# Performance work log

Measured on AMD Instinct MI355X. Metric: run time of the kernel, lower is better.

## Reference

```python
import jax, jax.numpy as jnp
import numpy as np

H = 16          # num_heads
DK = 64         # k_dim_head
DV = 64         # v_dim_head
DIM = 1024      # model dim (= H*DK = H*DV)


def _split_heads(x, h):
    # ... T (H d) -> ... H T d
    x = x.reshape(x.shape[:-1] + (h, -1))
    return jnp.swapaxes(x, -2, -3)


def _merge_heads(x):
    # ... H T d -> ... T (H d)
    x = jnp.swapaxes(x, -2, -3)
    return x.reshape(x.shape[:-2] + (-1,))


def setup_inputs() -> dict:
    key = jax.random.key(0)
    ks = jax.random.split(key, 8)
    B, T = 2, 2048
    q = jax.random.normal(ks[0], (B, T, DIM), dtype=jnp.float32)
    k = jax.random.normal(ks[1], (B, T, DIM), dtype=jnp.float32)
    v = jax.random.normal(ks[2], (B, T, DIM), dtype=jnp.float32)
    # causal boolean mask [T, T] (True = attend)
    mask = jnp.tril(jnp.ones((T, T), dtype=bool))
    s = 1.0 / np.sqrt(DIM)
    # weights stored as [in, out] so projection is x @ W (== torch Linear, no bias)
    Wq = jax.random.normal(ks[3], (DIM, H * DK), dtype=jnp.float32) * s
    Wk = jax.random.normal(ks[4], (DIM, H * DK), dtype=jnp.float32) * s
    Wv = jax.random.normal(ks[5], (DIM, H * DV), dtype=jnp.float32) * s
    Wo = jax.random.normal(ks[6], (H * DV, DIM), dtype=jnp.float32) * s
    return {"q": q, "k": k, "v": v, "mask": mask,
            "Wq": Wq, "Wk": Wk, "Wv": Wv, "Wo": Wo}


def reference(q, k, v, mask, Wq, Wk, Wv, Wo):
    q_i = _split_heads(q @ Wq, H)                       # ... H T dk
    k_i = _split_heads(k @ Wk, H)                       # ... H T dk
    v_i = _split_heads(v @ Wv, H)                       # ... H T dv
    s_qk = jnp.einsum('...hik,...hjk->...hij', q_i, k_i) / jnp.sqrt(
        jnp.asarray(DK, dtype=q_i.dtype))               # ... H T T
    neg = -jnp.finfo(s_qk.dtype).max
    s_qk = jnp.where(mask, s_qk, neg)
    attn = jax.nn.softmax(s_qk, axis=-1)
    vals = jnp.einsum('...hij,...hjv->...hiv', attn, v_i)
    return _merge_heads(vals) @ Wo                      # ... T out_dim
```

## Files before the change

### kernel.cpp

```cpp
#include <hip/hip_runtime.h>
#include <hip/hip_bf16.h>
#include <stdint.h>

#define T_SEQ  2048
#define DMODEL 1024
#define NBATCH 2
#define NHEAD  16
#define DHEAD  64
#define MTOT   (NBATCH * T_SEQ)

typedef __attribute__((ext_vector_type(8))) short short8_t;
typedef __attribute__((ext_vector_type(4))) float f32x4;

typedef const __attribute__((address_space(1))) void* gas_t;
typedef __attribute__((address_space(3))) void* las_t;

__device__ __forceinline__ ushort f2bf(float f) {
    union { float f; uint32_t u; } cv; cv.f = f;
    uint32_t u = cv.u;
    return (ushort)((u + 0x7FFFu + ((u >> 16) & 1u)) >> 16);
}

__global__ __launch_bounds__(256) void convert_qkv_kernel(
        const float* __restrict__ q, const float* __restrict__ k,
        const float* __restrict__ v, ushort* __restrict__ outb) {
    const size_t per = (size_t)MTOT * DMODEL / 4;
    size_t idx = (size_t)blockIdx.x * 256 + threadIdx.x;
    int t = (int)(idx / per);
    size_t i = idx - (size_t)t * per;
    const float4* src = (const float4*)(t == 0 ? q : (t == 1 ? k : v));
    float4 val = src[i];
    ushort4 o;
    o.x = f2bf(val.x); o.y = f2bf(val.y); o.z = f2bf(val.z); o.w = f2bf(val.w);
    ((ushort4*)outb)[(size_t)t * per + i] = o;
}

__global__ __launch_bounds__(256) void convw_kernel(
        const float* __restrict__ Wq, const float* __restrict__ Wk,
        const float* __restrict__ Wv, const float* __restrict__ Wo,
        ushort* __restrict__ wt) {
    __shared__ float tile[32][33];
    int z = blockIdx.z;
    const float* W = z == 0 ? Wq : z == 1 ? Wk : z == 2 ? Wv : Wo;
    const float sc = (z == 0) ? 0.125f : 1.0f;
    ushort* out = wt + (size_t)z * DMODEL * DMODEL;
    int tx = threadIdx.x, ty = threadIdx.y;
    int k0 = blockIdx.x * 32, n0 = blockIdx.y * 32;
    #pragma unroll
    for (int i = 0; i < 4; i++)
        tile[ty + i * 8][tx] = W[(size_t)(k0 + ty + i * 8) * DMODEL + n0 + tx];
    __syncthreads();
    #pragma unroll
    for (int i = 0; i < 4; i++)
        out[(size_t)(n0 + ty + i * 8) * DMODEL + k0 + tx] = f2bf(tile[tx][ty + i * 8] * sc);
}

template <bool OUT_F32>
__global__ __launch_bounds__(256, 2) void gemm_bt_kernel(
        const ushort* __restrict__ Aall, const ushort* __restrict__ Btall,
        void* __restrict__ Call, int M, int N, int K) {
    const ushort* A  = Aall  + (size_t)blockIdx.z * M * K;
    const ushort* Bt = Btall + (size_t)blockIdx.z * N * K;

    __shared__ ushort As[128 * 32];
    __shared__ ushort Bs[128 * 32];

    const int tid  = threadIdx.x;
    const int lane = tid & 63;
    const int wid  = tid >> 6;
    const int wr = wid >> 1, wc = wid & 1;
    const int m_base = blockIdx.x * 128;
    const int n_base = blockIdx.y * 128;

    f32x4 acc[4][4] = {};

    const int srow = lane >> 2;
    const int scol = (lane & 3) * 8;

    for (int kk = 0; kk < K; kk += 32) {
        __syncthreads();
        #pragma unroll
        for (int i = 0; i < 2; i++) {
            int c = wid * 2 + i;
            const ushort* ga = A  + (size_t)(m_base + c * 16 + srow) * K + kk + scol;
            const ushort* gb = Bt + (size_t)(n_base + c * 16 + srow) * K + kk + scol;
            __builtin_amdgcn_global_load_lds((gas_t)ga, (las_t)(As + c * 512), 16, 0, 0);
            __builtin_amdgcn_global_load_lds((gas_t)gb, (las_t)(Bs + c * 512), 16, 0, 0);
        }
        __syncthreads();
        short8_t a[4], b[4];
        #pragma unroll
        for (int mt = 0; mt < 4; mt++)
            a[mt] = *(const short8_t*)(As + (wr * 64 + mt * 16 + (lane & 15)) * 32 + (lane >> 4) * 8);
        #pragma unroll
        for (int nt = 0; nt < 4; nt++)
            b[nt] = *(const short8_t*)(Bs + (wc * 64 + nt * 16 + (lane & 15)) * 32 + (lane >> 4) * 8);
        #pragma unroll
        for (int mt = 0; mt < 4; mt++)
            #pragma unroll
            for (int nt = 0; nt < 4; nt++)
                acc[mt][nt] = __builtin_amdgcn_mfma_f32_16x16x32_bf16(a[mt], b[nt], acc[mt][nt], 0, 0, 0);
    }

    const int row0 = m_base + wr * 64 + (lane >> 4) * 4;
    const int col0 = n_base + wc * 64 + (lane & 15);
    if constexpr (OUT_F32) {
        float* C = (float*)Call + (size_t)blockIdx.z * M * N;
        #pragma unroll
        for (int mt = 0; mt < 4; mt++)
            #pragma unroll
            for (int nt = 0; nt < 4; nt++)
                #pragma unroll
                for (int r = 0; r < 4; r++)
                    C[(size_t)(row0 + mt * 16 + r) * N + col0 + nt * 16] = acc[mt][nt][r];
    } else {
        ushort* C = (ushort*)Call + (size_t)blockIdx.z * M * N;
        #pragma unroll
        for (int mt = 0; mt < 4; mt++)
            #pragma unroll
            for (int nt = 0; nt < 4; nt++)
                #pragma unroll
                for (int r = 0; r < 4; r++)
                    C[(size_t)(row0 + mt * 16 + r) * N + col0 + nt * 16] = f2bf(acc[mt][nt][r]);
    }
}

__global__ __launch_bounds__(256, 2) void attn_kernel(
        const ushort* __restrict__ Qp, const ushort* __restrict__ Kp,
        const ushort* __restrict__ Vp, ushort* __restrict__ Op) {
    __shared__ ushort Ksh[64 * 72];
    __shared__ ushort Vts[64 * 72];
    __shared__ ushort Psh[4 * 16 * 72];

    const int tid = threadIdx.x, lane = tid & 63, w = tid >> 6;
    const int g = lane >> 4;
    const int m = lane & 15;
    const int bh = blockIdx.y;
    const int b = bh >> 4, h = bh & 15;

    const ushort* Qb = Qp + (size_t)(b * T_SEQ) * DMODEL + h * DHEAD;
    const ushort* Kb = Kp + (size_t)(b * T_SEQ) * DMODEL + h * DHEAD;
    const ushort* Vb = Vp + (size_t)(b * T_SEQ) * DMODEL + h * DHEAD;
    ushort* Ob = Op + (size_t)(b * T_SEQ) * DMODEL + h * DHEAD;

    const int qa = blockIdx.x;
    const int na = qa + 1;

    const int kr  = tid >> 3, kck = (tid & 7) * 8;
    const int kvp = tid & 31, dvc = tid >> 5;

    short8_t kreg0, kreg1, vreg0, vreg1;
    auto LOADKV = [&](int kv0) {
        kreg0 = *(const short8_t*)(Kb + (size_t)(kv0 + kr) * DMODEL + kck);
        kreg1 = *(const short8_t*)(Kb + (size_t)(kv0 + kr + 32) * DMODEL + kck);
        const ushort* vsrc = Vb + (size_t)(kv0 + kvp * 2) * DMODEL + dvc * 8;
        vreg0 = *(const short8_t*)(vsrc);
        vreg1 = *(const short8_t*)(vsrc + DMODEL);
    };

    int qi = qa, q0 = qa * 64;
    short8_t qf[2];
    #pragma unroll
    for (int kc = 0; kc < 2; kc++)
        qf[kc] = *(const short8_t*)(Qb + (size_t)(q0 + w * 16 + m) * DMODEL + kc * 32 + g * 8);

    f32x4 acc_o[4] = {};
    float mrun = -1e30f, lrun = 0.f;

    ushort* Pw = Psh + w * 16 * 72;

    auto WRITE_O = [&]() {
        #pragma unroll
        for (int r = 0; r < 4; r++) {
            float linv = 1.f / __shfl(lrun, g * 4 + r);
            int qrow = q0 + w * 16 + g * 4 + r;
            #pragma unroll
            for (int dt = 0; dt < 4; dt++)
                Ob[(size_t)qrow * DMODEL + dt * 16 + m] = f2bf(acc_o[dt][r] * linv);
        }
    };

    LOADKV(0);

    for (int tt = 0; tt < 33; ++tt) {
        if (tt == na) {
            WRITE_O();
            #pragma unroll
            for (int dt = 0; dt < 4; dt++) acc_o[dt] = f32x4{0.f, 0.f, 0.f, 0.f};
            mrun = -1e30f; lrun = 0.f;
            qi = 31 - qa; q0 = qi * 64;
            #pragma unroll
            for (int kc = 0; kc < 2; kc++)
                qf[kc] = *(const short8_t*)(Qb + (size_t)(q0 + w * 16 + m) * DMODEL + kc * 32 + g * 8);
        }
        const int t = (tt < na) ? tt : tt - na;
        const int kv0 = t * 64;
        const bool need_mask = (t == qi);

        __syncthreads();
        *(short8_t*)(Ksh + kr * 72 + kck) = kreg0;
        *(short8_t*)(Ksh + (kr + 32) * 72 + kck) = kreg1;
        #pragma unroll
        for (int d = 0; d < 8; d++) {
            uint32_t pk = (uint32_t)(ushort)vreg0[d] | ((uint32_t)(ushort)vreg1[d] << 16);
            *(uint32_t*)(Vts + (dvc * 8 + d) * 72 + kvp * 2) = pk;
        }
        __syncthreads();

        if (tt < 32) {
            int tn = tt + 1;
            LOADKV(((tn < na) ? tn : tn - na) * 64);
        }

        f32x4 s[4] = {};
        #pragma unroll
        for (int kvT = 0; kvT < 4; kvT++)
            #pragma unroll
            for (int kc = 0; kc < 2; kc++) {
                short8_t kf = *(const short8_t*)(Ksh + (kvT * 16 + m) * 72 + kc * 32 + g * 8);
                s[kvT] = __builtin_amdgcn_mfma_f32_16x16x32_bf16(kf, qf[kc], s[kvT], 0, 0, 0);
            }

        const int qg = q0 + w * 16 + m;
        float pmax = -1e30f;
        #pragma unroll
        for (int kvT = 0; kvT < 4; kvT++)
            #pragma unroll
            for (int r = 0; r < 4; r++) {
                float val = s[kvT][r];
                if (need_mask) {
                    int kv_g = kv0 + kvT * 16 + g * 4 + r;
                    if (kv_g > qg) val = -1e30f;
                }
                s[kvT][r] = val;
                pmax = fmaxf(pmax, val);
            }
        pmax = fmaxf(pmax, __shfl_xor(pmax, 16));
        pmax = fmaxf(pmax, __shfl_xor(pmax, 32));
        float mnew = fmaxf(mrun, pmax);
        float fac = __expf(mrun - mnew);
        mrun = mnew;
        float psum = 0.f;
        #pragma unroll
        for (int kvT = 0; kvT < 4; kvT++)
            #pragma unroll
            for (int r = 0; r < 4; r++) {
                float p = __expf(s[kvT][r] - mrun);
                s[kvT][r] = p;
                psum += p;
            }
        psum += __shfl_xor(psum, 16);
        psum += __shfl_xor(psum, 32);
        lrun = lrun * fac + psum;

        #pragma unroll
        for (int kvT = 0; kvT < 4; kvT++) {
            uint32_t lo = (uint32_t)f2bf(s[kvT][0]) | ((uint32_t)f2bf(s[kvT][1]) << 16);
            uint32_t hi = (uint32_t)f2bf(s[kvT][2]) | ((uint32_t)f2bf(s[kvT][3]) << 16);
            uint2 pk; pk.x = lo; pk.y = hi;
            *(uint2*)(Pw + m * 72 + kvT * 16 + g * 4) = pk;
        }

        #pragma unroll
        for (int r = 0; r < 4; r++) {
            float f = __shfl(fac, g * 4 + r);
            #pragma unroll
            for (int dt = 0; dt < 4; dt++) acc_o[dt][r] *= f;
        }

        short8_t pf[2];
        #pragma unroll
        for (int kc = 0; kc < 2; kc++)
            pf[kc] = *(const short8_t*)(Pw + m * 72 + kc * 32 + g * 8);
        #pragma unroll
        for (int dt = 0; dt < 4; dt++)
            #pragma unroll
            for (int kc = 0; kc < 2; kc++) {
                short8_t vf = *(const short8_t*)(Vts + (dt * 16 + m) * 72 + kc * 32 + g * 8);
                acc_o[dt] = __builtin_amdgcn_mfma_f32_16x16x32_bf16(pf[kc], vf, acc_o[dt], 0, 0, 0);
            }
    }
    WRITE_O();
}

extern "C" void kernel_launch(void* const* d_in, const int* in_sizes, int n_in,
                              void* d_out, int out_size, void* d_ws, size_t ws_size,
                              hipStream_t stream) {
    (void)in_sizes; (void)n_in; (void)out_size; (void)ws_size;
    const float* q  = (const float*)d_in[0];
    const float* k  = (const float*)d_in[1];
    const float* v  = (const float*)d_in[2];
    const float* Wq = (const float*)d_in[4];
    const float* Wk = (const float*)d_in[5];
    const float* Wv = (const float*)d_in[6];
    const float* Wo = (const float*)d_in[7];

    ushort* ws = (ushort*)d_ws;
    const size_t MK = (size_t)MTOT * DMODEL;
    const size_t NK = (size_t)DMODEL * DMODEL;
    ushort* qkvb = ws;
    ushort* wt   = ws + 3 * MK;
    ushort* qkvp = ws + 3 * MK + 4 * NK;
    ushort* Op   = ws;

    convert_qkv_kernel<<<dim3(12288), dim3(256), 0, stream>>>(q, k, v, qkvb);
    convw_kernel<<<dim3(32, 32, 4), dim3(32, 8), 0, stream>>>(Wq, Wk, Wv, Wo, wt);
    gemm_bt_kernel<false><<<dim3(32, 8, 3), dim3(256), 0, stream>>>(qkvb, wt, (void*)qkvp,
                                                                    MTOT, DMODEL, DMODEL);
    attn_kernel<<<dim3(16, 32), dim3(256), 0, stream>>>(qkvp, qkvp + MK, qkvp + 2 * MK, Op);
    gemm_bt_kernel<true><<<dim3(32, 8, 1), dim3(256), 0, stream>>>(Op, wt + 3 * NK, d_out,
                                                                   MTOT, DMODEL, DMODEL);
}
```

Baseline: 134.4 us.

## Restructure attention with 32-row query tiles, double-buffered swizzled LDS, lazy rescaling

The attention kernel now runs 128-thread blocks, each handling a 32-row query tile, with twice as many blocks. K/V tiles are double-buffered in XOR-swizzled LDS so only one barrier is needed per iteration and loads run two tiles ahead. Softmax switches to exp2 by folding log2(e) into the Q weight scale, and rescales the accumulator only when the running max rises by more than a threshold. MFMA sections are wrapped in s_setprio. Risks include more tile overhead per block and bounded-growth numerics from the lazy rescale.

```diff
diff --git a/kernel.cpp b/kernel.cpp
--- a/kernel.cpp
+++ b/kernel.cpp
@@ -42,7 +42,7 @@
     __shared__ float tile[32][33];
     int z = blockIdx.z;
     const float* W = z == 0 ? Wq : z == 1 ? Wk : z == 2 ? Wv : Wo;
-    const float sc = (z == 0) ? 0.125f : 1.0f;
+    const float sc = (z == 0) ? 0.18033688011f : 1.0f;
     ushort* out = wt + (size_t)z * DMODEL * DMODEL;
     int tx = threadIdx.x, ty = threadIdx.y;
     int k0 = blockIdx.x * 32, n0 = blockIdx.y * 32;
@@ -125,16 +125,16 @@
     }
 }
 
-__global__ __launch_bounds__(256, 2) void attn_kernel(
+__global__ __launch_bounds__(128, 2) void attn_kernel(
         const ushort* __restrict__ Qp, const ushort* __restrict__ Kp,
         const ushort* __restrict__ Vp, ushort* __restrict__ Op) {
-    __shared__ ushort Ksh[64 * 72];
-    __shared__ ushort Vts[64 * 72];
-    __shared__ ushort Psh[4 * 16 * 72];
+    __shared__ __attribute__((aligned(16))) ushort Ksh[2][64 * 64];
+    __shared__ __attribute__((aligned(16))) ushort Vts[2][64 * 64];
+    __shared__ __attribute__((aligned(16))) ushort Psh[2][16 * 72];
 
     const int tid = threadIdx.x, lane = tid & 63, w = tid >> 6;
-    const int g = lane >> 4;
-    const int m = lane & 15;
+    const int g = lane >> 4, m = lane & 15;
+    const int xo = (m & 7) * 8;
     const int bh = blockIdx.y;
     const int b = bh >> 4, h = bh & 15;
 
@@ -144,21 +144,36 @@
     ushort* Ob = Op + (size_t)(b * T_SEQ) * DMODEL + h * DHEAD;
 
     const int qa = blockIdx.x;
-    const int na = qa + 1;
-
-    const int kr  = tid >> 3, kck = (tid & 7) * 8;
-    const int kvp = tid & 31, dvc = tid >> 5;
-
-    short8_t kreg0, kreg1, vreg0, vreg1;
+    const int qiB = 63 - qa;
+    const int na = (qa >> 1) + 1;
+
+    const int kr = tid >> 3, kslot = tid & 7;
+    const int ksw = (kslot ^ (kr & 7)) * 8;
+    const int kvq = tid & 15, dvc = tid >> 4;
+
+    short8_t kk[4], vv[4];
     auto LOADKV = [&](int kv0) {
-        kreg0 = *(const short8_t*)(Kb + (size_t)(kv0 + kr) * DMODEL + kck);
-        kreg1 = *(const short8_t*)(Kb + (size_t)(kv0 + kr + 32) * DMODEL + kck);
-        const ushort* vsrc = Vb + (size_t)(kv0 + kvp * 2) * DMODEL + dvc * 8;
-        vreg0 = *(const short8_t*)(vsrc);
-        vreg1 = *(const short8_t*)(vsrc + DMODEL);
+        #pragma unroll
+        for (int i = 0; i < 4; i++)
+            kk[i] = *(const short8_t*)(Kb + (size_t)(kv0 + kr + 16 * i) * DMODEL + kslot * 8);
+        #pragma unroll
+        for (int i = 0; i < 4; i++)
+            vv[i] = *(const short8_t*)(Vb + (size_t)(kv0 + kvq * 4 + i) * DMODEL + dvc * 8);
     };
-
-    int qi = qa, q0 = qa * 64;
+    auto WRITEKV = [&](int buf) {
+        #pragma unroll
+        for (int i = 0; i < 4; i++)
+            *(short8_t*)(&Ksh[buf][(kr + 16 * i) * 64 + ksw]) = kk[i];
+        #pragma unroll
+        for (int dd = 0; dd < 8; dd++) {
+            uint32_t lo = (uint32_t)(ushort)vv[0][dd] | ((uint32_t)(ushort)vv[1][dd] << 16);
+            uint32_t hi = (uint32_t)(ushort)vv[2][dd] | ((uint32_t)(ushort)vv[3][dd] << 16);
+            uint2 pk; pk.x = lo; pk.y = hi;
+            *(uint2*)(&Vts[buf][(dvc * 8 + dd) * 64 + (((kvq >> 1) ^ dd) * 8) + (kvq & 1) * 4]) = pk;
+        }
+    };
+
+    int qi = qa, q0 = qa * 32;
     short8_t qf[2];
     #pragma unroll
     for (int kc = 0; kc < 2; kc++)
@@ -166,8 +181,7 @@
 
     f32x4 acc_o[4] = {};
     float mrun = -1e30f, lrun = 0.f;
-
-    ushort* Pw = Psh + w * 16 * 72;
+    ushort* Pw = Psh[w];
 
     auto WRITE_O = [&]() {
         #pragma unroll
@@ -179,8 +193,11 @@
                 Ob[(size_t)qrow * DMODEL + dt * 16 + m] = f2bf(acc_o[dt][r] * linv);
         }
     };
-
-    LOADKV(0);
+    auto TILE = [&](int t) { return (t < na) ? t : t - na; };
+
+    LOADKV(TILE(0) * 64);
+    WRITEKV(0);
+    LOADKV(TILE(1) * 64);
 
     for (int tt = 0; tt < 33; ++tt) {
         if (tt == na) {
@@ -188,38 +205,32 @@
             #pragma unroll
             for (int dt = 0; dt < 4; dt++) acc_o[dt] = f32x4{0.f, 0.f, 0.f, 0.f};
             mrun = -1e30f; lrun = 0.f;
-            qi = 31 - qa; q0 = qi * 64;
+            qi = qiB; q0 = qi * 32;
             #pragma unroll
             for (int kc = 0; kc < 2; kc++)
                 qf[kc] = *(const short8_t*)(Qb + (size_t)(q0 + w * 16 + m) * DMODEL + kc * 32 + g * 8);
         }
-        const int t = (tt < na) ? tt : tt - na;
+        const int t = TILE(tt);
         const int kv0 = t * 64;
-        const bool need_mask = (t == qi);
+        const bool need_mask = (t == (qi >> 1));
+        const int cur = tt & 1;
 
         __syncthreads();
-        *(short8_t*)(Ksh + kr * 72 + kck) = kreg0;
-        *(short8_t*)(Ksh + (kr + 32) * 72 + kck) = kreg1;
-        #pragma unroll
-        for (int d = 0; d < 8; d++) {
-            uint32_t pk = (uint32_t)(ushort)vreg0[d] | ((uint32_t)(ushort)vreg1[d] << 16);
-            *(uint32_t*)(Vts + (dvc * 8 + d) * 72 + kvp * 2) = pk;
-        }
-        __syncthreads();
-
-        if (tt < 32) {
-            int tn = tt + 1;
-            LOADKV(((tn < na) ? tn : tn - na) * 64);
+        if (tt + 1 < 33) {
+            WRITEKV(cur ^ 1);
+            if (tt + 2 < 33) LOADKV(TILE(tt + 2) * 64);
         }
 
         f32x4 s[4] = {};
+        __builtin_amdgcn_s_setprio(1);
         #pragma unroll
         for (int kvT = 0; kvT < 4; kvT++)
             #pragma unroll
             for (int kc = 0; kc < 2; kc++) {
-                short8_t kf = *(const short8_t*)(Ksh + (kvT * 16 + m) * 72 + kc * 32 + g * 8);
+                short8_t kf = *(const short8_t*)(&Ksh[cur][(kvT * 16 + m) * 64 + ((kc * 32 + g * 8) ^ xo)]);
                 s[kvT] = __builtin_amdgcn_mfma_f32_16x16x32_bf16(kf, qf[kc], s[kvT], 0, 0, 0);
             }
+        __builtin_amdgcn_s_setprio(0);
 
         const int qg = q0 + w * 16 + m;
         float pmax = -1e30f;
@@ -237,21 +248,30 @@
             }
         pmax = fmaxf(pmax, __shfl_xor(pmax, 16));
         pmax = fmaxf(pmax, __shfl_xor(pmax, 32));
-        float mnew = fmaxf(mrun, pmax);
-        float fac = __expf(mrun - mnew);
-        mrun = mnew;
+        if (!__all(pmax <= mrun + 8.f)) {
+            float mnew = fmaxf(mrun, pmax);
+            float fac = exp2f(mrun - mnew);
+            mrun = mnew;
+            lrun *= fac;
+            #pragma unroll
+            for (int r = 0; r < 4; r++) {
+                float f = __shfl(fac, g * 4 + r);
+                #pragma unroll
+                for (int dt = 0; dt < 4; dt++) acc_o[dt][r] *= f;
+            }
+        }
         float psum = 0.f;
         #pragma unroll
         for (int kvT = 0; kvT < 4; kvT++)
             #pragma unroll
             for (int r = 0; r < 4; r++) {
-                float p = __expf(s[kvT][r] - mrun);
+                float p = exp2f(s[kvT][r] - mrun);
                 s[kvT][r] = p;
                 psum += p;
             }
         psum += __shfl_xor(psum, 16);
         psum += __shfl_xor(psum, 32);
-        lrun = lrun * fac + psum;
+        lrun += psum;
 
         #pragma unroll
         for (int kvT = 0; kvT < 4; kvT++) {
@@ -261,24 +281,19 @@
             *(uint2*)(Pw + m * 72 + kvT * 16 + g * 4) = pk;
         }
 
-        #pragma unroll
-        for (int r = 0; r < 4; r++) {
-            float f = __shfl(fac, g * 4 + r);
-            #pragma unroll
-            for (int dt = 0; dt < 4; dt++) acc_o[dt][r] *= f;
-        }
-
         short8_t pf[2];
         #pragma unroll
         for (int kc = 0; kc < 2; kc++)
             pf[kc] = *(const short8_t*)(Pw + m * 72 + kc * 32 + g * 8);
+        __builtin_amdgcn_s_setprio(1);
         #pragma unroll
         for (int dt = 0; dt < 4; dt++)
             #pragma unroll
             for (int kc = 0; kc < 2; kc++) {
-                short8_t vf = *(const short8_t*)(Vts + (dt * 16 + m) * 72 + kc * 32 + g * 8);
+                short8_t vf = *(const short8_t*)(&Vts[cur][(dt * 16 + m) * 64 + ((kc * 32 + g * 8) ^ xo)]);
                 acc_o[dt] = __builtin_amdgcn_mfma_f32_16x16x32_bf16(pf[kc], vf, acc_o[dt], 0, 0, 0);
             }
+        __builtin_amdgcn_s_setprio(0);
     }
     WRITE_O();
 }
@@ -307,7 +322,7 @@
     convw_kernel<<<dim3(32, 32, 4), dim3(32, 8), 0, stream>>>(Wq, Wk, Wv, Wo, wt);
     gemm_bt_kernel<false><<<dim3(32, 8, 3), dim3(256), 0, stream>>>(qkvb, wt, (void*)qkvp,
                                                                     MTOT, DMODEL, DMODEL);
-    attn_kernel<<<dim3(16, 32), dim3(256), 0, stream>>>(qkvp, qkvp + MK, qkvp + 2 * MK, Op);
+    attn_kernel<<<dim3(32, 32), dim3(128), 0, stream>>>(qkvp, qkvp + MK, qkvp + 2 * MK, Op);
     gemm_bt_kernel<true><<<dim3(32, 8, 1), dim3(256), 0, stream>>>(Op, wt + 3 * NK, d_out,
                                                                    MTOT, DMODEL, DMODEL);
 }
```

Result: slower. 168.8 us (+25.6%).

## Double-buffer K/V in LDS, use exp2 softmax with lazy rescaling and MFMA priority

Applied to the files above, without the earlier changes.

Splits the K/V shared-memory tiles into two buffers, so the next tile is written while the current one is consumed and one barrier per iteration is dropped. The softmax scale is folded into Wq with log2(e), so exp2f replaces __expf. The running-max rescale of the output accumulator is skipped unless some row's max grows by more than 8, which can leave P values up to 2^8 before bf16 rounding. s_setprio raises wave priority around the MFMA blocks. Double buffering doubles the K/V LDS footprint, which could affect occupancy.

```diff
diff --git a/kernel.cpp b/kernel.cpp
--- a/kernel.cpp
+++ b/kernel.cpp
@@ -42,7 +42,7 @@
     __shared__ float tile[32][33];
     int z = blockIdx.z;
     const float* W = z == 0 ? Wq : z == 1 ? Wk : z == 2 ? Wv : Wo;
-    const float sc = (z == 0) ? 0.125f : 1.0f;
+    const float sc = (z == 0) ? 0.18033688011f : 1.0f;
     ushort* out = wt + (size_t)z * DMODEL * DMODEL;
     int tx = threadIdx.x, ty = threadIdx.y;
     int k0 = blockIdx.x * 32, n0 = blockIdx.y * 32;
@@ -128,9 +128,9 @@
 __global__ __launch_bounds__(256, 2) void attn_kernel(
         const ushort* __restrict__ Qp, const ushort* __restrict__ Kp,
         const ushort* __restrict__ Vp, ushort* __restrict__ Op) {
-    __shared__ ushort Ksh[64 * 72];
-    __shared__ ushort Vts[64 * 72];
-    __shared__ ushort Psh[4 * 16 * 72];
+    __shared__ __attribute__((aligned(16))) ushort Ksh[2][64 * 72];
+    __shared__ __attribute__((aligned(16))) ushort Vts[2][64 * 72];
+    __shared__ __attribute__((aligned(16))) ushort Psh[4][16 * 72];
 
     const int tid = threadIdx.x, lane = tid & 63, w = tid >> 6;
     const int g = lane >> 4;
@@ -157,6 +157,15 @@
         vreg0 = *(const short8_t*)(vsrc);
         vreg1 = *(const short8_t*)(vsrc + DMODEL);
     };
+    auto WRITEKV = [&](int buf) {
+        *(short8_t*)(&Ksh[buf][kr * 72 + kck]) = kreg0;
+        *(short8_t*)(&Ksh[buf][(kr + 32) * 72 + kck]) = kreg1;
+        #pragma unroll
+        for (int d = 0; d < 8; d++) {
+            uint32_t pk = (uint32_t)(ushort)vreg0[d] | ((uint32_t)(ushort)vreg1[d] << 16);
+            *(uint32_t*)(&Vts[buf][(dvc * 8 + d) * 72 + kvp * 2]) = pk;
+        }
+    };
 
     int qi = qa, q0 = qa * 64;
     short8_t qf[2];
@@ -166,8 +175,7 @@
 
     f32x4 acc_o[4] = {};
     float mrun = -1e30f, lrun = 0.f;
-
-    ushort* Pw = Psh + w * 16 * 72;
+    ushort* Pw = Psh[w];
 
     auto WRITE_O = [&]() {
         #pragma unroll
@@ -179,8 +187,11 @@
                 Ob[(size_t)qrow * DMODEL + dt * 16 + m] = f2bf(acc_o[dt][r] * linv);
         }
     };
-
-    LOADKV(0);
+    auto TILE = [&](int t) { return (t < na) ? t : t - na; };
+
+    LOADKV(TILE(0) * 64);
+    WRITEKV(0);
+    LOADKV(TILE(1) * 64);
 
     for (int tt = 0; tt < 33; ++tt) {
         if (tt == na) {
@@ -193,33 +204,27 @@
             for (int kc = 0; kc < 2; kc++)
                 qf[kc] = *(const short8_t*)(Qb + (size_t)(q0 + w * 16 + m) * DMODEL + kc * 32 + g * 8);
         }
-        const int t = (tt < na) ? tt : tt - na;
+        const int t = TILE(tt);
         const int kv0 = t * 64;
         const bool need_mask = (t == qi);
+        const int cur = tt & 1;
 
         __syncthreads();
-        *(short8_t*)(Ksh + kr * 72 + kck) = kreg0;
-        *(short8_t*)(Ksh + (kr + 32) * 72 + kck) = kreg1;
-        #pragma unroll
-        for (int d = 0; d < 8; d++) {
-            uint32_t pk = (uint32_t)(ushort)vreg0[d] | ((uint32_t)(ushort)vreg1[d] << 16);
-            *(uint32_t*)(Vts + (dvc * 8 + d) * 72 + kvp * 2) = pk;
-        }
-        __syncthreads();
-
-        if (tt < 32) {
-            int tn = tt + 1;
-            LOADKV(((tn < na) ? tn : tn - na) * 64);
+        if (tt + 1 < 33) {
+            WRITEKV(cur ^ 1);
+            if (tt + 2 < 33) LOADKV(TILE(tt + 2) * 64);
         }
 
         f32x4 s[4] = {};
+        __builtin_amdgcn_s_setprio(1);
         #pragma unroll
         for (int kvT = 0; kvT < 4; kvT++)
             #pragma unroll
             for (int kc = 0; kc < 2; kc++) {
-                short8_t kf = *(const short8_t*)(Ksh + (kvT * 16 + m) * 72 + kc * 32 + g * 8);
+                short8_t kf = *(const short8_t*)(&Ksh[cur][(kvT * 16 + m) * 72 + kc * 32 + g * 8]);
                 s[kvT] = __builtin_amdgcn_mfma_f32_16x16x32_bf16(kf, qf[kc], s[kvT], 0, 0, 0);
             }
+        __builtin_amdgcn_s_setprio(0);
 
         const int qg = q0 + w * 16 + m;
         float pmax = -1e30f;
@@ -237,21 +242,30 @@
             }
         pmax = fmaxf(pmax, __shfl_xor(pmax, 16));
         pmax = fmaxf(pmax, __shfl_xor(pmax, 32));
-        float mnew = fmaxf(mrun, pmax);
-        float fac = __expf(mrun - mnew);
-        mrun = mnew;
+        if (!__all(pmax <= mrun + 8.f)) {
+            float mnew = fmaxf(mrun, pmax);
+            float fac = exp2f(mrun - mnew);
+            mrun = mnew;
+            lrun *= fac;
+            #pragma unroll
+            for (int r = 0; r < 4; r++) {
+                float f = __shfl(fac, g * 4 + r);
+                #pragma unroll
+                for (int dt = 0; dt < 4; dt++) acc_o[dt][r] *= f;
+            }
+        }
         float psum = 0.f;
         #pragma unroll
         for (int kvT = 0; kvT < 4; kvT++)
             #pragma unroll
             for (int r = 0; r < 4; r++) {
-                float p = __expf(s[kvT][r] - mrun);
+                float p = exp2f(s[kvT][r] - mrun);
                 s[kvT][r] = p;
                 psum += p;
             }
         psum += __shfl_xor(psum, 16);
         psum += __shfl_xor(psum, 32);
-        lrun = lrun * fac + psum;
+        lrun += psum;
 
         #pragma unroll
         for (int kvT = 0; kvT < 4; kvT++) {
@@ -261,24 +275,19 @@
             *(uint2*)(Pw + m * 72 + kvT * 16 + g * 4) = pk;
         }
 
-        #pragma unroll
-        for (int r = 0; r < 4; r++) {
-            float f = __shfl(fac, g * 4 + r);
-            #pragma unroll
-            for (int dt = 0; dt < 4; dt++) acc_o[dt][r] *= f;
-        }
-
         short8_t pf[2];
         #pragma unroll
         for (int kc = 0; kc < 2; kc++)
             pf[kc] = *(const short8_t*)(Pw + m * 72 + kc * 32 + g * 8);
+        __builtin_amdgcn_s_setprio(1);
         #pragma unroll
         for (int dt = 0; dt < 4; dt++)
             #pragma unroll
             for (int kc = 0; kc < 2; kc++) {
-                short8_t vf = *(const short8_t*)(Vts + (dt * 16 + m) * 72 + kc * 32 + g * 8);
+                short8_t vf = *(const short8_t*)(&Vts[cur][(dt * 16 + m) * 72 + kc * 32 + g * 8]);
                 acc_o[dt] = __builtin_amdgcn_mfma_f32_16x16x32_bf16(pf[kc], vf, acc_o[dt], 0, 0, 0);
             }
+        __builtin_amdgcn_s_setprio(0);
     }
     WRITE_O();
 }
```

Measured after the change: 138.2 us. 1.03x slower.
